# Performance work log

Measured on AMD Instinct MI355X. Metric: run time of the kernel, lower is better.

The kernel has to match this reference:

```python
import jax, jax.numpy as jnp
import numpy as np

B, S, D = 4, 2048, 1024
H, DQ, DK, DV = 16, 64, 64, 64


def setup_inputs() -> dict:
    key = jax.random.key(0)
    ks = jax.random.split(key, 8)
    q = jax.random.normal(ks[0], (B, S, D), dtype=jnp.float32)
    k = jax.random.normal(ks[1], (B, S, D), dtype=jnp.float32)
    v = jax.random.normal(ks[2], (B, S, D), dtype=jnp.float32)
    scale = 0.02
    Wq = jax.random.normal(ks[3], (H, D, DQ), dtype=jnp.float32) * scale
    Wk = jax.random.normal(ks[4], (H, D, DK), dtype=jnp.float32) * scale
    Wv = jax.random.normal(ks[5], (H, D, DV), dtype=jnp.float32) * scale
    Wo = jax.random.normal(ks[6], (D, D), dtype=jnp.float32) * scale
    bo = jax.random.normal(ks[7], (D,), dtype=jnp.float32) * scale
    return {"q": q, "k": k, "v": v, "Wq": Wq, "Wk": Wk, "Wv": Wv, "Wo": Wo, "bo": bo}


def reference(q, k, v, Wq, Wk, Wv, Wo, bo):
    # Per-head projections (batched over heads instead of the Python loop).
    Q = jnp.einsum('bsd,hdq->bhsq', q, Wq)  # [B,H,S,DQ]
    K = jnp.einsum('bsd,hdk->bhsk', k, Wk)  # [B,H,S,DK]
    V = jnp.einsum('bsd,hdv->bhsv', v, Wv)  # [B,H,S,DV]
    # Scaled dot-product scores; original divides by sqrt(d_query).
    scores = jnp.einsum('bhsq,bhtq->bhst', Q, K) / jnp.sqrt(jnp.float32(Q.shape[-1]))
    # Causal mask (tril buffer registered when is_masked=True).
    causal = jnp.tril(jnp.ones((S, S), dtype=bool))
    scores = jnp.where(causal, scores, -jnp.inf)
    attn = jax.nn.softmax(scores, axis=-1)
    out = jnp.einsum('bhst,bhtv->bhsv', attn, V)  # [B,H,S,DV]
    # Concatenate heads along feature dim: [B,S,H*DV] == [B,S,D].
    out = out.transpose(0, 2, 1, 3).reshape(B, S, H * DV)
    # Output projection (dropout is identity with p=0 / eval mode).
    return out @ Wo.T + bo
```

## Files before the change

kernel.cpp:

```cpp
#include <hip/hip_runtime.h>

typedef __bf16 bf16_t;
typedef __bf16 bf16x8 __attribute__((ext_vector_type(8)));
typedef float f32x4 __attribute__((ext_vector_type(4)));

#define MFMA16(a, b, c) __builtin_amdgcn_mfma_f32_16x16x32_bf16((a), (b), (c), 0, 0, 0)

#define GLOAD_LDS16(gsrc, ldst)                                                      \
  __builtin_amdgcn_global_load_lds(                                                  \
      (const __attribute__((address_space(1))) uint32_t*)(const void*)(gsrc),        \
      (__attribute__((address_space(3))) uint32_t*)(void*)(ldst), 16, 0, 0)

constexpr int B_ = 4, S_ = 2048, D_ = 1024, H_ = 16, DH_ = 64;

__global__ __launch_bounds__(256) void prep_w(const float* __restrict__ W,
                                              bf16_t* __restrict__ Wt) {
  __shared__ float tile[64][65];
  int h = blockIdx.y, k0 = blockIdx.x * 64, tid = threadIdx.x;
  int r = tid >> 2, cb = (tid & 3) * 16;
  const float* src = W + h * (D_ * DH_) + (k0 + r) * DH_ + cb;
  float4 f0 = ((const float4*)src)[0];
  float4 f1 = ((const float4*)src)[1];
  float4 f2 = ((const float4*)src)[2];
  float4 f3 = ((const float4*)src)[3];
  tile[r][cb + 0] = f0.x;  tile[r][cb + 1] = f0.y;  tile[r][cb + 2] = f0.z;  tile[r][cb + 3] = f0.w;
  tile[r][cb + 4] = f1.x;  tile[r][cb + 5] = f1.y;  tile[r][cb + 6] = f1.z;  tile[r][cb + 7] = f1.w;
  tile[r][cb + 8] = f2.x;  tile[r][cb + 9] = f2.y;  tile[r][cb + 10] = f2.z; tile[r][cb + 11] = f2.w;
  tile[r][cb + 12] = f3.x; tile[r][cb + 13] = f3.y; tile[r][cb + 14] = f3.z; tile[r][cb + 15] = f3.w;
  __syncthreads();
  int j = tid >> 2, kb = (tid & 3) * 16;
  bf16_t tmp[16] __attribute__((aligned(16)));
#pragma unroll
  for (int c = 0; c < 16; ++c) tmp[c] = (bf16_t)tile[kb + c][j];
  bf16_t* dst = Wt + (h * 64 + j) * D_ + k0 + kb;
  *(uint4*)dst = ((uint4*)tmp)[0];
  *(uint4*)(dst + 8) = ((uint4*)tmp)[1];
}

__global__ __launch_bounds__(256) void prep_wo(const float* __restrict__ W,
                                               bf16_t* __restrict__ Wt) {
  int i = (blockIdx.x * 256 + threadIdx.x) * 4;
  float4 f = *(const float4*)&W[i];
  bf16_t t[4] __attribute__((aligned(8)));
  t[0] = (bf16_t)f.x; t[1] = (bf16_t)f.y; t[2] = (bf16_t)f.z; t[3] = (bf16_t)f.w;
  *(uint2*)&Wt[i] = *(uint2*)t;
}

__global__ __launch_bounds__(256) void gemm_qkv(
    const float* __restrict__ Aq, const float* __restrict__ Ak, const float* __restrict__ Av,
    const bf16_t* __restrict__ Wt_all,
    bf16_t* __restrict__ Qp, bf16_t* __restrict__ Kp, bf16_t* __restrict__ Vt) {
  __shared__ __attribute__((aligned(16))) float  Afl[128 * 32];
  __shared__ __attribute__((aligned(16))) bf16_t Bl[128 * 32];
  int gz = blockIdx.z;
  const float* A = gz == 0 ? Aq : (gz == 1 ? Ak : Av);
  const bf16_t* W = Wt_all + gz * (D_ * D_);
  int m0 = blockIdx.x * 128, n0 = blockIdx.y * 128;
  int tid = threadIdx.x, lane = tid & 63, w = tid >> 6;
  int wm = (w & 1) * 64, wn = (w >> 1) * 64;
  int l15 = lane & 15, quad = lane >> 4;
  int sw = l15 & 7;

  int ar = lane >> 3;
  int acol = ((lane & 7) ^ ar) * 4;
  int br = lane >> 2;
  int bcol = (lane & 3) * 8;

  f32x4 acc[4][4] = {};

  for (int kk = 0; kk < D_; kk += 32) {
    const float* abase = A + (size_t)m0 * D_ + kk + acol;
#pragma unroll
    for (int it = 0; it < 4; ++it) {
      int chunk = it * 4 + w;
      GLOAD_LDS16(abase + (size_t)(chunk * 8 + ar) * D_, &Afl[chunk * 256]);
    }
    const bf16_t* bbase = W + (size_t)n0 * D_ + kk + bcol;
#pragma unroll
    for (int ib = 0; ib < 2; ++ib) {
      int chunk = ib * 4 + w;
      GLOAD_LDS16(bbase + (size_t)(chunk * 16 + br) * D_, &Bl[chunk * 512]);
    }
    __syncthreads();

    bf16x8 af[4], bf[4];
#pragma unroll
    for (int i = 0; i < 4; ++i) {
      int ra = wm + i * 16 + l15;
      float4 f0 = *(const float4*)&Afl[ra * 32 + (((quad * 2) ^ sw) << 2)];
      float4 f1 = *(const float4*)&Afl[ra * 32 + (((quad * 2 + 1) ^ sw) << 2)];
      bf16x8 a;
      a[0] = (bf16_t)f0.x; a[1] = (bf16_t)f0.y; a[2] = (bf16_t)f0.z; a[3] = (bf16_t)f0.w;
      a[4] = (bf16_t)f1.x; a[5] = (bf16_t)f1.y; a[6] = (bf16_t)f1.z; a[7] = (bf16_t)f1.w;
      af[i] = a;
      bf[i] = *(const bf16x8*)&Bl[(wn + i * 16 + l15) * 32 + quad * 8];
    }
#pragma unroll
    for (int i = 0; i < 4; ++i)
#pragma unroll
      for (int j = 0; j < 4; ++j) acc[i][j] = MFMA16(af[i], bf[j], acc[i][j]);
    __syncthreads();
  }

  if (gz < 2) {
    bf16_t* Out = gz == 0 ? Qp : Kp;
#pragma unroll
    for (int i = 0; i < 4; ++i)
#pragma unroll
      for (int j = 0; j < 4; ++j)
#pragma unroll
        for (int r = 0; r < 4; ++r) {
          int m = m0 + wm + i * 16 + quad * 4 + r;
          int n = n0 + wn + j * 16 + l15;
          Out[(size_t)m * D_ + n] = (bf16_t)acc[i][j][r];
        }
  } else {
#pragma unroll
    for (int i = 0; i < 4; ++i)
#pragma unroll
      for (int j = 0; j < 4; ++j) {
        int m = m0 + wm + i * 16 + quad * 4;
        int b = m >> 11, sl = m & (S_ - 1);
        int n = n0 + wn + j * 16 + l15;
        int h = n >> 6, d = n & 63;
        bf16_t t4[4] __attribute__((aligned(8)));
        t4[0] = (bf16_t)acc[i][j][0]; t4[1] = (bf16_t)acc[i][j][1];
        t4[2] = (bf16_t)acc[i][j][2]; t4[3] = (bf16_t)acc[i][j][3];
        *(uint2*)&Vt[((size_t)(b * H_ + h) * DH_ + d) * S_ + sl] = *(uint2*)t4;
      }
  }
}

__global__ __launch_bounds__(256, 4) void attn(
    const bf16_t* __restrict__ Qp, const bf16_t* __restrict__ Kp,
    const bf16_t* __restrict__ Vt, bf16_t* __restrict__ Ob) {
  __shared__ __attribute__((aligned(16))) bf16_t Kl[2][4096];
  __shared__ __attribute__((aligned(16))) bf16_t Vl[2][4096];
  __shared__ __attribute__((aligned(16))) bf16_t Pt[4][1024];

  int bidx = blockIdx.x;
  int bh = blockIdx.y, b = bh >> 4, h = bh & 15;
  int tid = threadIdx.x, lane = tid & 63, w = tid >> 6;
  int l15 = lane & 15, quad = lane >> 4;
  int sw = l15 & 7;
  const float csc = 0.125f * 1.44269504f;

  bf16_t* Ptw = Pt[w];
  int rr = lane >> 3, cc = lane & 7;
  int colsw = ((cc ^ rr) * 8);

#pragma unroll 1
  for (int ph = 0; ph < 2; ++ph) {
    int qt = ph ? 31 - bidx : bidx;

    int sg_base = qt * 64 + w * 16;
    const bf16_t* qptr = Qp + (size_t)(b * S_ + sg_base + l15) * D_ + h * DH_ + quad * 8;
    bf16x8 qa0 = *(const bf16x8*)qptr;
    bf16x8 qa1 = *(const bf16x8*)(qptr + 32);

    f32x4 o[4] = {};
    float m = -3.0e38f, l = 0.f;

    __syncthreads();

    {
      const bf16_t* kb = Kp + (size_t)(b * S_) * D_ + h * DH_ + colsw;
      const bf16_t* vb = Vt + (size_t)(bh * DH_) * S_ + colsw;
#pragma unroll
      for (int ro = 0; ro < 2; ++ro) {
        int tl = (ro * 4 + w) * 8 + rr;
        GLOAD_LDS16(kb + (size_t)tl * D_, &Kl[0][(ro * 4 + w) * 512]);
        GLOAD_LDS16(vb + (size_t)tl * S_, &Vl[0][(ro * 4 + w) * 512]);
      }
    }

    for (int jt = 0; jt <= qt; ++jt) {
      __syncthreads();

      if (jt < qt) {
        int nb = (jt + 1) & 1;
        const bf16_t* kb = Kp + (size_t)(b * S_ + (jt + 1) * 64) * D_ + h * DH_ + colsw;
        const bf16_t* vb = Vt + (size_t)(bh * DH_) * S_ + (jt + 1) * 64 + colsw;
#pragma unroll
        for (int ro = 0; ro < 2; ++ro) {
          int tl = (ro * 4 + w) * 8 + rr;
          GLOAD_LDS16(kb + (size_t)tl * D_, &Kl[nb][(ro * 4 + w) * 512]);
          GLOAD_LDS16(vb + (size_t)tl * S_, &Vl[nb][(ro * 4 + w) * 512]);
        }
      }

      const bf16_t* Kb = Kl[jt & 1];
      const bf16_t* Vb = Vl[jt & 1];
      bool diag = (jt == qt);

      f32x4 sc[4];
#pragma unroll
      for (int n = 0; n < 4; ++n) {
        if (diag && n > w) {
          sc[n] = (f32x4){-3.0e38f, -3.0e38f, -3.0e38f, -3.0e38f};
          continue;
        }
        bf16x8 kb0 = *(const bf16x8*)&Kb[(n * 16 + l15) * 64 + ((quad) ^ sw) * 8];
        bf16x8 kb1 = *(const bf16x8*)&Kb[(n * 16 + l15) * 64 + ((quad + 4) ^ sw) * 8];
        f32x4 z = {};
        z = MFMA16(kb0, qa0, z);
        z = MFMA16(kb1, qa1, z);
        if (diag && n == w) {
#pragma unroll
          for (int r = 0; r < 4; ++r)
            if (quad * 4 + r > l15) z[r] = -3.0e38f;
        }
        sc[n] = z;
      }

      float mx = -3.0e38f;
#pragma unroll
      for (int n = 0; n < 4; ++n)
#pragma unroll
        for (int r = 0; r < 4; ++r) mx = fmaxf(mx, sc[n][r]);
      mx = fmaxf(mx, __shfl_xor(mx, 16));
      mx = fmaxf(mx, __shfl_xor(mx, 32));
      float mnew = fmaxf(m, mx);
      float alpha = __builtin_amdgcn_exp2f((m - mnew) * csc);
      m = mnew;
      float msc = mnew * csc;

      float rs = 0.f;
      uint32_t pk[4][2];
#pragma unroll
      for (int n = 0; n < 4; ++n) {
        bf16_t pb[4] __attribute__((aligned(8)));
#pragma unroll
        for (int r = 0; r < 4; ++r) {
          float p = __builtin_amdgcn_exp2f(sc[n][r] * csc - msc);
          rs += p;
          pb[r] = (bf16_t)p;
        }
        pk[n][0] = ((uint32_t*)pb)[0];
        pk[n][1] = ((uint32_t*)pb)[1];
      }
      rs += __shfl_xor(rs, 16);
      rs += __shfl_xor(rs, 32);
      l = l * alpha + rs;

#pragma unroll
      for (int n = 0; n < 4; ++n) {
        int off = l15 * 64 + ((n * 2 + (quad >> 1)) ^ sw) * 8 + (quad & 1) * 4;
        *(uint2*)&Ptw[off] = make_uint2(pk[n][0], pk[n][1]);
      }
#pragma unroll
      for (int n = 0; n < 4; ++n) o[n] *= alpha;

      asm volatile("s_waitcnt lgkmcnt(0)" ::: "memory");

      bf16x8 pb0 = *(const bf16x8*)&Ptw[l15 * 64 + ((quad) ^ sw) * 8];
      bf16x8 pb1 = *(const bf16x8*)&Ptw[l15 * 64 + ((quad + 4) ^ sw) * 8];

#pragma unroll
      for (int n = 0; n < 4; ++n) {
        bf16x8 va0 = *(const bf16x8*)&Vb[(n * 16 + l15) * 64 + ((quad) ^ sw) * 8];
        bf16x8 va1 = *(const bf16x8*)&Vb[(n * 16 + l15) * 64 + ((quad + 4) ^ sw) * 8];
        o[n] = MFMA16(va0, pb0, o[n]);
        o[n] = MFMA16(va1, pb1, o[n]);
      }
    }

    float inv = 1.0f / l;
    asm volatile("s_waitcnt lgkmcnt(0)" ::: "memory");
#pragma unroll
    for (int n = 0; n < 4; ++n) {
      bf16_t t4[4] __attribute__((aligned(8)));
#pragma unroll
      for (int r = 0; r < 4; ++r) t4[r] = (bf16_t)(o[n][r] * inv);
      int off = l15 * 64 + ((n * 2 + (quad >> 1)) ^ sw) * 8 + (quad & 1) * 4;
      *(uint2*)&Ptw[off] = *(uint2*)t4;
    }
    asm volatile("s_waitcnt lgkmcnt(0)" ::: "memory");
    {
      int sg = qt * 64 + w * 16 + l15;
      bf16x8 r0 = *(const bf16x8*)&Ptw[l15 * 64 + ((quad * 2) ^ sw) * 8];
      bf16x8 r1 = *(const bf16x8*)&Ptw[l15 * 64 + ((quad * 2 + 1) ^ sw) * 8];
      bf16_t* op = Ob + (size_t)(b * S_ + sg) * D_ + h * DH_ + quad * 16;
      *(bf16x8*)op = r0;
      *(bf16x8*)(op + 8) = r1;
    }
  }
}

__global__ __launch_bounds__(256) void gemm_out(
    const bf16_t* __restrict__ Ab, const bf16_t* __restrict__ Wot,
    const float* __restrict__ bo, float* __restrict__ Out) {
  __shared__ __attribute__((aligned(16))) bf16_t Al[128 * 32];
  __shared__ __attribute__((aligned(16))) bf16_t Bl[128 * 32];
  int m0 = blockIdx.x * 128, n0 = blockIdx.y * 128;
  int tid = threadIdx.x, lane = tid & 63, w = tid >> 6;
  int wm = (w & 1) * 64, wn = (w >> 1) * 64;
  int l15 = lane & 15, quad = lane >> 4;
  int br = lane >> 2, bcol = (lane & 3) * 8;

  f32x4 acc[4][4] = {};

  for (int kk = 0; kk < D_; kk += 32) {
    const bf16_t* abase = Ab + (size_t)m0 * D_ + kk + bcol;
    const bf16_t* bbase = Wot + (size_t)n0 * D_ + kk + bcol;
#pragma unroll
    for (int ib = 0; ib < 2; ++ib) {
      int chunk = ib * 4 + w;
      GLOAD_LDS16(abase + (size_t)(chunk * 16 + br) * D_, &Al[chunk * 512]);
      GLOAD_LDS16(bbase + (size_t)(chunk * 16 + br) * D_, &Bl[chunk * 512]);
    }
    __syncthreads();
    bf16x8 af[4], bf[4];
#pragma unroll
    for (int i = 0; i < 4; ++i) {
      af[i] = *(const bf16x8*)&Al[(wm + i * 16 + l15) * 32 + quad * 8];
      bf[i] = *(const bf16x8*)&Bl[(wn + i * 16 + l15) * 32 + quad * 8];
    }
#pragma unroll
    for (int i = 0; i < 4; ++i)
#pragma unroll
      for (int j = 0; j < 4; ++j) acc[i][j] = MFMA16(af[i], bf[j], acc[i][j]);
    __syncthreads();
  }

#pragma unroll
  for (int j = 0; j < 4; ++j) {
    int n = n0 + wn + j * 16 + l15;
    float bias = bo[n];
#pragma unroll
    for (int i = 0; i < 4; ++i)
#pragma unroll
      for (int r = 0; r < 4; ++r) {
        int m = m0 + wm + i * 16 + quad * 4 + r;
        Out[(size_t)m * D_ + n] = acc[i][j][r] + bias;
      }
  }
}

extern "C" void kernel_launch(void* const* d_in, const int* in_sizes, int n_in,
                              void* d_out, int out_size, void* d_ws, size_t ws_size,
                              hipStream_t stream) {
  const float* q = (const float*)d_in[0];
  const float* k = (const float*)d_in[1];
  const float* v = (const float*)d_in[2];
  const float* Wq = (const float*)d_in[3];
  const float* Wk = (const float*)d_in[4];
  const float* Wv = (const float*)d_in[5];
  const float* Wo = (const float*)d_in[6];
  const float* bo = (const float*)d_in[7];
  float* out = (float*)d_out;

  bf16_t* wsb = (bf16_t*)d_ws;
  const size_t MD = (size_t)8192 * 1024;
  bf16_t* Wqt = wsb;
  bf16_t* Wot = wsb + 3 * (size_t)(D_ * D_);
  bf16_t* Qp  = wsb + 4 * (size_t)(D_ * D_);
  bf16_t* Kp  = Qp + MD;
  bf16_t* Vt  = Kp + MD;
  bf16_t* Ab  = Vt + MD;

  prep_w<<<dim3(16, 16), 256, 0, stream>>>(Wq, Wqt);
  prep_w<<<dim3(16, 16), 256, 0, stream>>>(Wk, Wqt + (size_t)(D_ * D_));
  prep_w<<<dim3(16, 16), 256, 0, stream>>>(Wv, Wqt + 2 * (size_t)(D_ * D_));
  prep_wo<<<1024, 256, 0, stream>>>(Wo, Wot);
  gemm_qkv<<<dim3(64, 8, 3), 256, 0, stream>>>(q, k, v, Wqt, Qp, Kp, Vt);
  attn<<<dim3(16, 64), 256, 0, stream>>>(Qp, Kp, Vt, Ab);
  gemm_out<<<dim3(64, 8), 256, 0, stream>>>(Ab, Wot, bo, out);
}
```

Before: 352.1 us.

## Pre-convert inputs to bf16 and load GEMM fragments directly from global memory

A new pass converts q, k and v to bf16 before the QKV projection. Both GEMMs drop their LDS staging and barriers, and each wave instead loads its MFMA fragments straight from global memory into registers, double-buffered across k-steps, with launch bounds requesting three blocks per CU. The aim is to remove LDS round-trips, syncthreads stalls and in-loop fp32-to-bf16 conversion. In exchange there is an extra conversion pass over the inputs, more redundant global/L2 traffic because fragments are no longer shared across waves through LDS, and more register pressure. The bf16 input copies reuse the attention-output buffer, which is safe only because the attention kernel writes that buffer after the QKV GEMM has consumed it.

```diff
diff --git a/kernel.cpp b/kernel.cpp
--- a/kernel.cpp
+++ b/kernel.cpp
@@ -46,60 +46,66 @@
   *(uint2*)&Wt[i] = *(uint2*)t;
 }
 
-__global__ __launch_bounds__(256) void gemm_qkv(
-    const float* __restrict__ Aq, const float* __restrict__ Ak, const float* __restrict__ Av,
-    const bf16_t* __restrict__ Wt_all,
+__global__ __launch_bounds__(256) void cvt_bf16(const float* __restrict__ q,
+                                                const float* __restrict__ k,
+                                                const float* __restrict__ v,
+                                                bf16_t* __restrict__ qb,
+                                                bf16_t* __restrict__ kb,
+                                                bf16_t* __restrict__ vb) {
+  int z = blockIdx.y;
+  const float* src = z == 0 ? q : (z == 1 ? k : v);
+  bf16_t* dst = z == 0 ? qb : (z == 1 ? kb : vb);
+  size_t i = ((size_t)blockIdx.x * 256 + threadIdx.x) * 8;
+  float4 f0 = *(const float4*)&src[i];
+  float4 f1 = *(const float4*)&src[i + 4];
+  bf16_t t[8] __attribute__((aligned(16)));
+  t[0] = (bf16_t)f0.x; t[1] = (bf16_t)f0.y; t[2] = (bf16_t)f0.z; t[3] = (bf16_t)f0.w;
+  t[4] = (bf16_t)f1.x; t[5] = (bf16_t)f1.y; t[6] = (bf16_t)f1.z; t[7] = (bf16_t)f1.w;
+  *(uint4*)&dst[i] = *(uint4*)t;
+}
+
+__global__ __launch_bounds__(256, 3) void gemm_qkv(
+    const bf16_t* __restrict__ qb, const bf16_t* __restrict__ kb,
+    const bf16_t* __restrict__ vb, const bf16_t* __restrict__ Wt_all,
     bf16_t* __restrict__ Qp, bf16_t* __restrict__ Kp, bf16_t* __restrict__ Vt) {
-  __shared__ __attribute__((aligned(16))) float  Afl[128 * 32];
-  __shared__ __attribute__((aligned(16))) bf16_t Bl[128 * 32];
   int gz = blockIdx.z;
-  const float* A = gz == 0 ? Aq : (gz == 1 ? Ak : Av);
-  const bf16_t* W = Wt_all + gz * (D_ * D_);
+  const bf16_t* A = gz == 0 ? qb : (gz == 1 ? kb : vb);
+  const bf16_t* W = Wt_all + (size_t)gz * (D_ * D_);
   int m0 = blockIdx.x * 128, n0 = blockIdx.y * 128;
-  int tid = threadIdx.x, lane = tid & 63, w = tid >> 6;
+  int lane = threadIdx.x & 63, w = threadIdx.x >> 6;
   int wm = (w & 1) * 64, wn = (w >> 1) * 64;
   int l15 = lane & 15, quad = lane >> 4;
-  int sw = l15 & 7;
-
-  int ar = lane >> 3;
-  int acol = ((lane & 7) ^ ar) * 4;
-  int br = lane >> 2;
-  int bcol = (lane & 3) * 8;
+
+  const bf16_t* pa[4];
+  const bf16_t* pb[4];
+#pragma unroll
+  for (int i = 0; i < 4; ++i) {
+    pa[i] = A + (size_t)(m0 + wm + i * 16 + l15) * D_ + quad * 8;
+    pb[i] = W + (size_t)(n0 + wn + i * 16 + l15) * D_ + quad * 8;
+  }
 
   f32x4 acc[4][4] = {};
-
-  for (int kk = 0; kk < D_; kk += 32) {
-    const float* abase = A + (size_t)m0 * D_ + kk + acol;
-#pragma unroll
-    for (int it = 0; it < 4; ++it) {
-      int chunk = it * 4 + w;
-      GLOAD_LDS16(abase + (size_t)(chunk * 8 + ar) * D_, &Afl[chunk * 256]);
-    }
-    const bf16_t* bbase = W + (size_t)n0 * D_ + kk + bcol;
-#pragma unroll
-    for (int ib = 0; ib < 2; ++ib) {
-      int chunk = ib * 4 + w;
-      GLOAD_LDS16(bbase + (size_t)(chunk * 16 + br) * D_, &Bl[chunk * 512]);
-    }
-    __syncthreads();
-
-    bf16x8 af[4], bf[4];
-#pragma unroll
-    for (int i = 0; i < 4; ++i) {
-      int ra = wm + i * 16 + l15;
-      float4 f0 = *(const float4*)&Afl[ra * 32 + (((quad * 2) ^ sw) << 2)];
-      float4 f1 = *(const float4*)&Afl[ra * 32 + (((quad * 2 + 1) ^ sw) << 2)];
-      bf16x8 a;
-      a[0] = (bf16_t)f0.x; a[1] = (bf16_t)f0.y; a[2] = (bf16_t)f0.z; a[3] = (bf16_t)f0.w;
-      a[4] = (bf16_t)f1.x; a[5] = (bf16_t)f1.y; a[6] = (bf16_t)f1.z; a[7] = (bf16_t)f1.w;
-      af[i] = a;
-      bf[i] = *(const bf16x8*)&Bl[(wn + i * 16 + l15) * 32 + quad * 8];
-    }
-#pragma unroll
-    for (int i = 0; i < 4; ++i)
-#pragma unroll
-      for (int j = 0; j < 4; ++j) acc[i][j] = MFMA16(af[i], bf[j], acc[i][j]);
-    __syncthreads();
+  bf16x8 af[2][4], bfr[2][4];
+#pragma unroll
+  for (int i = 0; i < 4; ++i) {
+    af[0][i] = *(const bf16x8*)pa[i];
+    bfr[0][i] = *(const bf16x8*)pb[i];
+  }
+
+#pragma unroll
+  for (int t = 0; t < 32; ++t) {
+    int cur = t & 1, nxt = cur ^ 1;
+    if (t < 31) {
+#pragma unroll
+      for (int i = 0; i < 4; ++i) {
+        af[nxt][i] = *(const bf16x8*)(pa[i] + (t + 1) * 32);
+        bfr[nxt][i] = *(const bf16x8*)(pb[i] + (t + 1) * 32);
+      }
+    }
+#pragma unroll
+    for (int i = 0; i < 4; ++i)
+#pragma unroll
+      for (int j = 0; j < 4; ++j) acc[i][j] = MFMA16(af[cur][i], bfr[cur][j], acc[i][j]);
   }
 
   if (gz < 2) {
@@ -287,40 +293,44 @@
   }
 }
 
-__global__ __launch_bounds__(256) void gemm_out(
+__global__ __launch_bounds__(256, 3) void gemm_out(
     const bf16_t* __restrict__ Ab, const bf16_t* __restrict__ Wot,
     const float* __restrict__ bo, float* __restrict__ Out) {
-  __shared__ __attribute__((aligned(16))) bf16_t Al[128 * 32];
-  __shared__ __attribute__((aligned(16))) bf16_t Bl[128 * 32];
   int m0 = blockIdx.x * 128, n0 = blockIdx.y * 128;
-  int tid = threadIdx.x, lane = tid & 63, w = tid >> 6;
+  int lane = threadIdx.x & 63, w = threadIdx.x >> 6;
   int wm = (w & 1) * 64, wn = (w >> 1) * 64;
   int l15 = lane & 15, quad = lane >> 4;
-  int br = lane >> 2, bcol = (lane & 3) * 8;
+
+  const bf16_t* pa[4];
+  const bf16_t* pb[4];
+#pragma unroll
+  for (int i = 0; i < 4; ++i) {
+    pa[i] = Ab + (size_t)(m0 + wm + i * 16 + l15) * D_ + quad * 8;
+    pb[i] = Wot + (size_t)(n0 + wn + i * 16 + l15) * D_ + quad * 8;
+  }
 
   f32x4 acc[4][4] = {};
-
-  for (int kk = 0; kk < D_; kk += 32) {
-    const bf16_t* abase = Ab + (size_t)m0 * D_ + kk + bcol;
-    const bf16_t* bbase = Wot + (size_t)n0 * D_ + kk + bcol;
-#pragma unroll
-    for (int ib = 0; ib < 2; ++ib) {
-      int chunk = ib * 4 + w;
-      GLOAD_LDS16(abase + (size_t)(chunk * 16 + br) * D_, &Al[chunk * 512]);
-      GLOAD_LDS16(bbase + (size_t)(chunk * 16 + br) * D_, &Bl[chunk * 512]);
-    }
-    __syncthreads();
-    bf16x8 af[4], bf[4];
-#pragma unroll
-    for (int i = 0; i < 4; ++i) {
-      af[i] = *(const bf16x8*)&Al[(wm + i * 16 + l15) * 32 + quad * 8];
-      bf[i] = *(const bf16x8*)&Bl[(wn + i * 16 + l15) * 32 + quad * 8];
-    }
-#pragma unroll
-    for (int i = 0; i < 4; ++i)
-#pragma unroll
-      for (int j = 0; j < 4; ++j) acc[i][j] = MFMA16(af[i], bf[j], acc[i][j]);
-    __syncthreads();
+  bf16x8 af[2][4], bfr[2][4];
+#pragma unroll
+  for (int i = 0; i < 4; ++i) {
+    af[0][i] = *(const bf16x8*)pa[i];
+    bfr[0][i] = *(const bf16x8*)pb[i];
+  }
+
+#pragma unroll
+  for (int t = 0; t < 32; ++t) {
+    int cur = t & 1, nxt = cur ^ 1;
+    if (t < 31) {
+#pragma unroll
+      for (int i = 0; i < 4; ++i) {
+        af[nxt][i] = *(const bf16x8*)(pa[i] + (t + 1) * 32);
+        bfr[nxt][i] = *(const bf16x8*)(pb[i] + (t + 1) * 32);
+      }
+    }
+#pragma unroll
+    for (int i = 0; i < 4; ++i)
+#pragma unroll
+      for (int j = 0; j < 4; ++j) acc[i][j] = MFMA16(af[cur][i], bfr[cur][j], acc[i][j]);
   }
 
 #pragma unroll
@@ -358,12 +368,16 @@
   bf16_t* Kp  = Qp + MD;
   bf16_t* Vt  = Kp + MD;
   bf16_t* Ab  = Vt + MD;
+  bf16_t* qb  = Ab;
+  bf16_t* kb  = Ab + MD;
+  bf16_t* vb  = kb + MD;
 
   prep_w<<<dim3(16, 16), 256, 0, stream>>>(Wq, Wqt);
   prep_w<<<dim3(16, 16), 256, 0, stream>>>(Wk, Wqt + (size_t)(D_ * D_));
   prep_w<<<dim3(16, 16), 256, 0, stream>>>(Wv, Wqt + 2 * (size_t)(D_ * D_));
   prep_wo<<<1024, 256, 0, stream>>>(Wo, Wot);
-  gemm_qkv<<<dim3(64, 8, 3), 256, 0, stream>>>(q, k, v, Wqt, Qp, Kp, Vt);
+  cvt_bf16<<<dim3(4096, 3), 256, 0, stream>>>(q, k, v, qb, kb, vb);
+  gemm_qkv<<<dim3(64, 8, 3), 256, 0, stream>>>(qb, kb, vb, Wqt, Qp, Kp, Vt);
   attn<<<dim3(16, 64), 256, 0, stream>>>(Qp, Kp, Vt, Ab);
   gemm_out<<<dim3(64, 8), 256, 0, stream>>>(Ab, Wot, bo, out);
 }
```

Result: slower. 509.0 us (+44.6%).
